# Kernel tuning notes

Measured on AMD Instinct MI355X. Metric: run time of the kernel, lower is better.

Reference implementation:

```python
import jax, jax.numpy as jnp
import numpy as np

VOCAB = 32000
DIM = 1024
DFF = 4096
NLLM = 3
B, S = 2, 2048
THRESH = 0.98
EPS = 1e-8


def setup_inputs() -> dict:
    key = jax.random.key(0)
    ks = jax.random.split(key, 5)
    x = jax.random.randint(ks[0], (B, S), 0, VOCAB)
    emb = 0.02 * jax.random.normal(ks[1], (VOCAB, DIM), jnp.float32)
    ln_g = jnp.ones((NLLM, DIM), jnp.float32)
    ln_b = jnp.zeros((NLLM, DIM), jnp.float32)
    W1 = 0.002 * jax.random.normal(ks[2], (NLLM, DIM, DFF), jnp.float32)
    b1 = jnp.zeros((NLLM, DFF), jnp.float32)
    W2 = 0.002 * jax.random.normal(ks[3], (NLLM, DFF, DIM), jnp.float32)
    b2 = jnp.zeros((NLLM, DIM), jnp.float32)
    W_out = (1.0 / np.sqrt(DIM)) * jax.random.normal(ks[4], (VOCAB, DIM), jnp.float32)
    return dict(x=x, emb=emb, ln_g=ln_g, ln_b=ln_b, W1=W1, b1=b1, W2=W2, b2=b2, W_out=W_out)


def _layernorm(h, g, b):
    m = jnp.mean(h, axis=-1, keepdims=True)
    v = jnp.var(h, axis=-1, keepdims=True)
    return (h - m) * jax.lax.rsqrt(v + 1e-5) * g + b


def reference(x, emb, ln_g, ln_b, W1, b1, W2, b2, W_out):
    # Cascaded early-exit ensemble. The torch code physically re-packs surviving
    # tokens; since each LLM block here is per-token (residual MLP), a masked
    # formulation computes identical per-token math and is jit-compatible.
    Bb, Ss = x.shape
    T = Bb * Ss
    h = emb[x.reshape(T)]                      # [T, D] token embeddings
    active = jnp.ones((T,), dtype=bool)
    final = jnp.zeros((T, VOCAB), dtype=h.dtype)
    for i in range(NLLM):                      # fixed, small number of LLMs
        hn = _layernorm(h, ln_g[i], ln_b[i])
        mlp = jax.nn.gelu(hn @ W1[i] + b1[i]) @ W2[i] + b2[i]
        h_out = h + mlp                        # [T, D]
        logits = h_out @ W_out.T               # [T, V] shared output head
        cos = jnp.sum(h * h_out, axis=-1) / (
            jnp.linalg.norm(h, axis=-1) * jnp.linalg.norm(h_out, axis=-1) + EPS)
        is_last = (i == NLLM - 1)
        should_exit = cos >= THRESH
        take = active if is_last else (active & should_exit)
        final = jnp.where(take[:, None], logits, final)   # scatter logits for exiting tokens
        active = active & (~take)
        h = jnp.where(active[:, None], h_out, h)          # continuing tokens carry h_out forward
    return final.reshape(Bb, Ss, VOCAB)
```

## Files before the change

kernel.cpp:

```cpp
#include <hip/hip_runtime.h>
#include <hip/hip_bf16.h>
#include <stdint.h>

constexpr int TK   = 4096;
constexpr int DIMC = 1024;
constexpr int DFFC = 4096;
constexpr int VOC  = 32000;
constexpr int NL   = 3;

typedef __attribute__((ext_vector_type(8))) short bf16x8;
typedef __attribute__((ext_vector_type(8))) _Float16 half8;
typedef __attribute__((ext_vector_type(4))) float f32x4;
using u16 = unsigned short;

__device__ __forceinline__ u16 f2bf(float f) {
  unsigned int u = __float_as_uint(f);
  u += 0x7FFF + ((u >> 16) & 1);
  return (u16)(u >> 16);
}

__device__ __forceinline__ void split16(float v, u16& hi, u16& lo) {
  _Float16 a = (_Float16)v;
  _Float16 b = (_Float16)(v - (float)a);
  hi = __builtin_bit_cast(u16, a);
  lo = __builtin_bit_cast(u16, b);
}

__device__ __forceinline__ float gelu_f(float x) {
  float x3 = x * x * x;
  return 0.5f * x * (1.0f + tanhf(0.7978845608028654f * (x + 0.044715f * x3)));
}

__device__ __forceinline__ void gll16(const void* g, void* l) {
  __builtin_amdgcn_global_load_lds(
      (const __attribute__((address_space(1))) unsigned int*)g,
      (__attribute__((address_space(3))) unsigned int*)l, 16, 0, 0);
}

__global__ __launch_bounds__(256) void k_init(const int* __restrict__ x,
    const float* __restrict__ emb, float* __restrict__ h,
    int* __restrict__ surv, int* __restrict__ cnts) {
  const int t = blockIdx.x, tid = threadIdx.x;
  if (t == 0 && tid < 16) cnts[tid] = (tid == 12) ? TK : 0;
  if (tid == 0) surv[t] = t;
  const int tok = x[t];
  ((float4*)(h + (size_t)t * DIMC))[tid] =
      ((const float4*)(emb + (size_t)tok * DIMC))[tid];
}

__global__ __launch_bounds__(256) void k_ln(const float* __restrict__ h,
    const int* __restrict__ surv, const int* __restrict__ pM,
    const float* __restrict__ g, const float* __restrict__ b,
    u16* __restrict__ hn1, u16* __restrict__ hn2) {
  const int bidx = blockIdx.x;
  if (bidx >= *pM) return;
  const int t = surv[bidx];
  const int tid = threadIdx.x;
  const int lane = tid & 63, wid = tid >> 6;
  __shared__ float sm[4];
  float4 v = ((const float4*)(h + (size_t)t * DIMC))[tid];
  float s = v.x + v.y + v.z + v.w;
#pragma unroll
  for (int o = 32; o; o >>= 1) s += __shfl_down(s, o);
  if (lane == 0) sm[wid] = s;
  __syncthreads();
  const float mean = (sm[0] + sm[1] + sm[2] + sm[3]) * (1.0f / DIMC);
  __syncthreads();
  float4 d;
  d.x = v.x - mean; d.y = v.y - mean; d.z = v.z - mean; d.w = v.w - mean;
  float q = d.x * d.x + d.y * d.y + d.z * d.z + d.w * d.w;
#pragma unroll
  for (int o = 32; o; o >>= 1) q += __shfl_down(q, o);
  if (lane == 0) sm[wid] = q;
  __syncthreads();
  const float var = (sm[0] + sm[1] + sm[2] + sm[3]) * (1.0f / DIMC);
  const float rstd = 1.0f / sqrtf(var + 1e-5f);
  float4 gg = ((const float4*)g)[tid];
  float4 bb = ((const float4*)b)[tid];
  float o4[4];
  o4[0] = (d.x * rstd * gg.x + bb.x) * 16.f;
  o4[1] = (d.y * rstd * gg.y + bb.y) * 16.f;
  o4[2] = (d.z * rstd * gg.z + bb.z) * 16.f;
  o4[3] = (d.w * rstd * gg.w + bb.w) * 16.f;
  ushort4 u1, u2;
  split16(o4[0], u1.x, u2.x); split16(o4[1], u1.y, u2.y);
  split16(o4[2], u1.z, u2.z); split16(o4[3], u1.w, u2.w);
  ((ushort4*)(hn1 + (size_t)bidx * DIMC))[tid] = u1;
  ((ushort4*)(hn2 + (size_t)bidx * DIMC))[tid] = u2;
}

__global__ __launch_bounds__(256) void k_splitw(const float* __restrict__ W,
    int K, int N, u16* __restrict__ O1, u16* __restrict__ O2) {
  __shared__ float t[32][33];
  const int bk = blockIdx.x * 32, bn = blockIdx.y * 32;
  const int lx = threadIdx.x & 31, ly = threadIdx.x >> 5;
#pragma unroll
  for (int i = 0; i < 32; i += 8)
    t[ly + i][lx] = W[(size_t)(bk + ly + i) * N + bn + lx];
  __syncthreads();
#pragma unroll
  for (int i = 0; i < 32; i += 8) {
    float v = t[lx][ly + i] * 256.f;
    u16 h1, h2; split16(v, h1, h2);
    const size_t o = (size_t)(bn + ly + i) * K + bk + lx;
    O1[o] = h1; O2[o] = h2;
  }
}

__global__ __launch_bounds__(256) void k_cvtb(const float* __restrict__ in,
    u16* __restrict__ o, int n4) {
  int i = blockIdx.x * blockDim.x + threadIdx.x;
  const int stride = gridDim.x * blockDim.x;
  for (; i < n4; i += stride) {
    float4 v = ((const float4*)in)[i];
    ushort4 u;
    u.x = f2bf(v.x); u.y = f2bf(v.y); u.z = f2bf(v.z); u.w = f2bf(v.w);
    ((ushort4*)o)[i] = u;
  }
}

template<int EPI, int LDK>
__global__ __launch_bounds__(256, 2) void k_mlp(
    const u16* __restrict__ wsb,
    int offA, int pstrA,
    int offB, int pstrB,
    const int* __restrict__ pM, int Kpart,
    const float* __restrict__ bias,
    u16* __restrict__ O1, u16* __restrict__ O2,
    float* __restrict__ PO, float osc)
{
  const int x = blockIdx.x & 7, g = blockIdx.x >> 3;
  const int rb = g & 31;
  int cb, z;
  if constexpr (EPI == 0) {
    cb = x * 4 + (g >> 5); z = 0;
  } else {
    const int cz = x * 2 + (g >> 5);
    cb = cz & 7; z = cz >> 3;
  }
  const int M = *pM;
  if (rb * 128 >= M) return;
  const int n0 = cb * 128;
  const int kz = z * Kpart;

  __shared__ u16 S[4 * 8192];
  const int tid = threadIdx.x, w = tid >> 6, l = tid & 63;
  const int lr16 = l & 15, hi = l >> 4;

  int offT;
  if (w == 0) offT = offA;
  else if (w == 1) offT = offA + pstrA;
  else if (w == 2) offT = offB;
  else offT = offB + pstrB;
  const int row0 = (w < 2) ? (rb * 128) : n0;
  const int gbase = offT + (row0 + lr16) * LDK + kz + hi * 8;

  const int wr = w >> 1, wc = w & 1;
  f32x4 acc[4][4];
#pragma unroll
  for (int mi = 0; mi < 4; ++mi)
#pragma unroll
    for (int ni = 0; ni < 4; ++ni) acc[mi][ni] = (f32x4){0.f, 0.f, 0.f, 0.f};

  const int NT = Kpart / 64;
  for (int kt = 0; kt < NT; ++kt) {
    __syncthreads();
#pragma unroll
    for (int s = 0; s < 16; ++s) {
      const int j = s >> 1, ks = s & 1;
      gll16(wsb + (size_t)(gbase + j * 16 * LDK + ks * 32 + kt * 64),
            (void*)&S[w * 8192 + (j * 2 + ks) * 512]);
    }
    __syncthreads();
#pragma unroll
    for (int ks = 0; ks < 2; ++ks) {
      half8 a1v[4], a2v[4], b1v[4], b2v[4];
#pragma unroll
      for (int mi = 0; mi < 4; ++mi) {
        const int sub = ((wr * 4 + mi) * 2 + ks) * 512 + l * 8;
        a1v[mi] = *(const half8*)&S[sub];
        a2v[mi] = *(const half8*)&S[8192 + sub];
      }
#pragma unroll
      for (int ni = 0; ni < 4; ++ni) {
        const int sub = ((wc * 4 + ni) * 2 + ks) * 512 + l * 8;
        b1v[ni] = *(const half8*)&S[16384 + sub];
        b2v[ni] = *(const half8*)&S[24576 + sub];
      }
      __builtin_amdgcn_s_setprio(1);
#pragma unroll
      for (int mi = 0; mi < 4; ++mi)
#pragma unroll
        for (int ni = 0; ni < 4; ++ni) {
          f32x4 c = acc[mi][ni];
          c = __builtin_amdgcn_mfma_f32_16x16x32_f16(a2v[mi], b1v[ni], c, 0, 0, 0);
          c = __builtin_amdgcn_mfma_f32_16x16x32_f16(a1v[mi], b2v[ni], c, 0, 0, 0);
          c = __builtin_amdgcn_mfma_f32_16x16x32_f16(a1v[mi], b1v[ni], c, 0, 0, 0);
          acc[mi][ni] = c;
        }
      __builtin_amdgcn_s_setprio(0);
    }
  }

#pragma unroll
  for (int mi = 0; mi < 4; ++mi)
#pragma unroll
    for (int ni = 0; ni < 4; ++ni) {
      const int n = n0 + wc * 64 + ni * 16 + lr16;
#pragma unroll
      for (int r = 0; r < 4; ++r) {
        const int m = rb * 128 + wr * 64 + mi * 16 + hi * 4 + r;
        float v = acc[mi][ni][r] * osc;
        if constexpr (EPI == 0) {
          v = gelu_f(v + bias[n]) * 64.f;
          u16 h1, h2; split16(v, h1, h2);
          O1[(size_t)m * DFFC + n] = h1;
          O2[(size_t)m * DFFC + n] = h2;
        } else {
          PO[(size_t)(z * TK + m) * DIMC + n] = v;
        }
      }
    }
}

__global__ __launch_bounds__(256) void k_decide(
    float* __restrict__ h, const float* __restrict__ p,
    const float* __restrict__ bias,
    const int* __restrict__ surv_in, int* __restrict__ surv_out,
    const int* __restrict__ pM, int* __restrict__ cnts,
    int* __restrict__ exit_idx, u16* __restrict__ hexit,
    int stage)
{
  const int bidx = blockIdx.x;
  if (bidx >= *pM) return;
  const int t = surv_in[bidx];
  const int tid = threadIdx.x;
  const int lane = tid & 63, wid = tid >> 6;
  __shared__ float sm[12];
  __shared__ int sif[2];
  float4 a  = ((const float4*)(h + (size_t)t * DIMC))[tid];
  float4 p0 = ((const float4*)(p + (size_t)bidx * DIMC))[tid];
  float4 p1 = ((const float4*)(p + (size_t)(TK + bidx) * DIMC))[tid];
  float4 bb = ((const float4*)bias)[tid];
  float4 o;
  o.x = a.x + p0.x + p1.x + bb.x;
  o.y = a.y + p0.y + p1.y + bb.y;
  o.z = a.z + p0.z + p1.z + bb.z;
  o.w = a.w + p0.w + p1.w + bb.w;
  float hh = a.x * a.x + a.y * a.y + a.z * a.z + a.w * a.w;
  float ho = a.x * o.x + a.y * o.y + a.z * o.z + a.w * o.w;
  float oo = o.x * o.x + o.y * o.y + o.z * o.z + o.w * o.w;
#pragma unroll
  for (int off = 32; off; off >>= 1) {
    hh += __shfl_down(hh, off);
    ho += __shfl_down(ho, off);
    oo += __shfl_down(oo, off);
  }
  if (lane == 0) { sm[wid] = hh; sm[4 + wid] = ho; sm[8 + wid] = oo; }
  __syncthreads();
  if (tid == 0) {
    int take;
    if (stage == NL - 1) take = 1;
    else {
      const float HH = sm[0] + sm[1] + sm[2] + sm[3];
      const float HO = sm[4] + sm[5] + sm[6] + sm[7];
      const float OO = sm[8] + sm[9] + sm[10] + sm[11];
      const float cosv = HO / (sqrtf(HH) * sqrtf(OO) + 1e-8f);
      take = (cosv >= 0.98f) ? 1 : 0;
    }
    int pos;
    if (take) {
      pos = atomicAdd(&cnts[stage], 1);
      exit_idx[pos] = t;
    } else {
      pos = atomicAdd(&cnts[4 + stage], 1);
      surv_out[pos] = t;
    }
    sif[0] = take; sif[1] = pos;
  }
  __syncthreads();
  if (sif[0]) {
    u16* dst = hexit + (size_t)sif[1] * DIMC;
    ushort4 u;
    u.x = f2bf(o.x); u.y = f2bf(o.y); u.z = f2bf(o.z); u.w = f2bf(o.w);
    ((ushort4*)dst)[tid] = u;
  } else {
    ((float4*)(h + (size_t)t * DIMC))[tid] = o;
  }
}

__global__ __launch_bounds__(512, 4) void k_logits(
    const u16* __restrict__ wsb, int offA, int offB,
    const int* __restrict__ pcnt,
    const int* __restrict__ exit_idx,
    float* __restrict__ out)
{
  const int x = blockIdx.x & 7, g = blockIdx.x >> 3;
  const int rb = g & 15;
  const int cb = x * 32 + (g >> 4);
  if (cb >= VOC / 128) return;
  const int cnt = *pcnt;
  if (rb * 256 >= cnt) return;
  const int n0 = cb * 128;

  __shared__ u16 S[2][12288];
  const int tid = threadIdx.x, w = tid >> 6, l = tid & 63;
  const int lr16 = l & 15, hi = l >> 4;

  int goff[3], loff[3];
#pragma unroll
  for (int q = 0; q < 3; ++q) {
    const int bi = w * 3 + q;
    if (bi < 16) {
      goff[q] = offA + (rb * 256 + bi * 16 + lr16) * DIMC + hi * 8;
      loff[q] = bi * 512;
    } else {
      const int j = bi - 16;
      goff[q] = offB + (n0 + j * 16 + lr16) * DIMC + hi * 8;
      loff[q] = 8192 + j * 512;
    }
  }

  const int wr = w >> 1, wc = w & 1;
  f32x4 acc[4][4];
#pragma unroll
  for (int mi = 0; mi < 4; ++mi)
#pragma unroll
    for (int ni = 0; ni < 4; ++ni) acc[mi][ni] = (f32x4){0.f, 0.f, 0.f, 0.f};

  auto STAGE = [&](int buf, int kt) {
#pragma unroll
    for (int q = 0; q < 3; ++q)
      gll16(wsb + (size_t)(goff[q] + kt * 32), (void*)&S[buf][loff[q]]);
  };

  STAGE(0, 0);
  STAGE(1, 1);
  const int NT = DIMC / 32;
  for (int kt = 0; kt < NT; ++kt) {
    const int cur = kt & 1;
    if (kt + 1 < NT) asm volatile("s_waitcnt vmcnt(3)" ::: "memory");
    else             asm volatile("s_waitcnt vmcnt(0)" ::: "memory");
    __builtin_amdgcn_s_barrier();
    bf16x8 aF[4], bF[4];
#pragma unroll
    for (int mi = 0; mi < 4; ++mi)
      aF[mi] = *(const bf16x8*)&S[cur][(wr * 4 + mi) * 512 + l * 8];
#pragma unroll
    for (int ni = 0; ni < 4; ++ni)
      bF[ni] = *(const bf16x8*)&S[cur][8192 + (wc * 4 + ni) * 512 + l * 8];
    __builtin_amdgcn_s_setprio(1);
#pragma unroll
    for (int mi = 0; mi < 4; ++mi)
#pragma unroll
      for (int ni = 0; ni < 4; ++ni)
        acc[mi][ni] = __builtin_amdgcn_mfma_f32_16x16x32_bf16(aF[mi], bF[ni], acc[mi][ni], 0, 0, 0);
    __builtin_amdgcn_s_setprio(0);
    asm volatile("s_waitcnt lgkmcnt(0)" ::: "memory");
    __builtin_amdgcn_s_barrier();
    if (kt + 2 < NT) STAGE(cur, kt + 2);
  }

  const int mvalid = cnt - rb * 256;
#pragma unroll
  for (int mi = 0; mi < 4; ++mi)
#pragma unroll
    for (int r = 0; r < 4; ++r) {
      const int mrow = wr * 64 + mi * 16 + hi * 4 + r;
      if (mrow < mvalid) {
        const int tok = exit_idx[rb * 256 + mrow];
        float* orow = out + (size_t)tok * VOC + n0 + wc * 64 + lr16;
#pragma unroll
        for (int ni = 0; ni < 4; ++ni)
          __builtin_nontemporal_store(acc[mi][ni][r], &orow[ni * 16]);
      }
    }
}

extern "C" void kernel_launch(void* const* d_in, const int* in_sizes, int n_in,
                              void* d_out, int out_size, void* d_ws, size_t ws_size,
                              hipStream_t stream)
{
  const int*   x    = (const int*)d_in[0];
  const float* emb  = (const float*)d_in[1];
  const float* ln_g = (const float*)d_in[2];
  const float* ln_b = (const float*)d_in[3];
  const float* W1   = (const float*)d_in[4];
  const float* b1   = (const float*)d_in[5];
  const float* W2   = (const float*)d_in[6];
  const float* b2   = (const float*)d_in[7];
  const float* Wout = (const float*)d_in[8];
  float* out = (float*)d_out;

  char* p = (char*)d_ws;
  size_t off = 0;
  auto alloc = [&](size_t bytes) -> void* {
    void* r = p + off;
    off += (bytes + 255) & ~(size_t)255;
    return r;
  };
  u16* wsb = (u16*)d_ws;
  float* h    = (float*)alloc((size_t)TK * DIMC * 4);
  float* pbuf = (float*)alloc((size_t)2 * TK * DIMC * 4);
  u16* hn1 = (u16*)pbuf;
  u16* hn2 = hn1 + (size_t)TK * DIMC;
  u16* act1 = (u16*)alloc((size_t)2 * TK * DFFC * 2);
  u16* act2 = act1 + (size_t)TK * DFFC;
  u16* Woutb = (u16*)alloc((size_t)VOC * DIMC * 2);
  u16* Wt = (u16*)alloc((size_t)2 * DFFC * DIMC * 2);
  u16* hexit = (u16*)alloc((size_t)TK * DIMC * 2);
  int* exit_idx = (int*)alloc((size_t)TK * 4);
  int* surv_a   = (int*)alloc((size_t)TK * 4);
  int* surv_b   = (int*)alloc((size_t)TK * 4);
  int* cnts     = (int*)alloc(64 * 4);

  const int offHn  = (int)(hn1  - wsb);
  const int offAct = (int)(act1 - wsb);
  const int offWob = (int)(Woutb- wsb);
  const int offWt  = (int)(Wt   - wsb);
  const int offHex = (int)(hexit- wsb);
  const int pstrHn  = TK * DIMC;
  const int pstrAct = TK * DFFC;
  const int pstrW   = DFFC * DIMC;

  k_init<<<TK, 256, 0, stream>>>(x, emb, h, surv_a, cnts);
  k_cvtb<<<2048, 256, 0, stream>>>(Wout, Woutb, VOC * DIMC / 4);
  int* surv_in  = surv_a;
  int* surv_out = surv_b;
  for (int i = 0; i < NL; ++i) {
    const int* pM = (i == 0) ? (cnts + 12) : (cnts + 4 + (i - 1));
    k_ln<<<TK, 256, 0, stream>>>(h, surv_in, pM, ln_g + i * DIMC, ln_b + i * DIMC, hn1, hn2);
    k_splitw<<<dim3(DIMC / 32, DFFC / 32), 256, 0, stream>>>(
        W1 + (size_t)i * DIMC * DFFC, DIMC, DFFC, Wt, Wt + (size_t)DFFC * DIMC);
    k_mlp<0, DIMC><<<1024, 256, 0, stream>>>(
        wsb, offHn, pstrHn, offWt, pstrW, pM, DIMC,
        b1 + (size_t)i * DFFC, act1, act2, nullptr, 1.f / 4096.f);
    k_splitw<<<dim3(DFFC / 32, DIMC / 32), 256, 0, stream>>>(
        W2 + (size_t)i * DFFC * DIMC, DFFC, DIMC, Wt, Wt + (size_t)DIMC * DFFC);
    k_mlp<1, DFFC><<<512, 256, 0, stream>>>(
        wsb, offAct, pstrAct, offWt, pstrW, pM, DFFC / 2,
        nullptr, nullptr, nullptr, pbuf, 1.f / 16384.f);
    k_decide<<<TK, 256, 0, stream>>>(h, pbuf, b2 + (size_t)i * DIMC,
        surv_in, surv_out, pM, cnts, exit_idx, hexit, i);
    k_logits<<<4096, 512, 0, stream>>>(wsb, offHex, offWob, cnts + i, exit_idx, out);
    int* tmp = surv_in; surv_in = surv_out; surv_out = tmp;
  }
}
```

Baseline: 1.461 ms.

## Double-buffer MLP GEMM shared-memory loads and vectorize weight split-transpose

The MLP GEMM kernel moves from a single 64-wide K stage with two full barriers to a double-buffered 32-wide K pipeline. The next tile's global-to-LDS loads are issued while MFMAs run on the current buffer, synchronised with explicit vmcnt/lgkmcnt waits and raw barriers. The weight split/transpose kernel now uses 64x64 tiles and writes ushort4 vectors instead of scalar u16 stores. This aims to hide load latency and cut store transactions, at the cost of more barriers per K step and delicate hand-written waitcnt ordering.

```diff
diff --git a/kernel.cpp b/kernel.cpp
--- a/kernel.cpp
+++ b/kernel.cpp
@@ -91,19 +91,28 @@
 
 __global__ __launch_bounds__(256) void k_splitw(const float* __restrict__ W,
     int K, int N, u16* __restrict__ O1, u16* __restrict__ O2) {
-  __shared__ float t[32][33];
-  const int bk = blockIdx.x * 32, bn = blockIdx.y * 32;
-  const int lx = threadIdx.x & 31, ly = threadIdx.x >> 5;
-#pragma unroll
-  for (int i = 0; i < 32; i += 8)
+  __shared__ float t[64][65];
+  const int bk = blockIdx.x * 64, bn = blockIdx.y * 64;
+  const int lx = threadIdx.x & 63, ly = threadIdx.x >> 6;
+#pragma unroll
+  for (int i = 0; i < 64; i += 4)
     t[ly + i][lx] = W[(size_t)(bk + ly + i) * N + bn + lx];
   __syncthreads();
-#pragma unroll
-  for (int i = 0; i < 32; i += 8) {
-    float v = t[lx][ly + i] * 256.f;
-    u16 h1, h2; split16(v, h1, h2);
-    const size_t o = (size_t)(bn + ly + i) * K + bk + lx;
-    O1[o] = h1; O2[o] = h2;
+  const int n4 = threadIdx.x >> 4;
+  const int kq = (threadIdx.x & 15) * 4;
+#pragma unroll
+  for (int j = 0; j < 4; ++j) {
+    const int n = j * 16 + n4;
+    ushort4 h1, h2;
+    {
+      float v0 = t[kq + 0][n] * 256.f, v1 = t[kq + 1][n] * 256.f;
+      float v2 = t[kq + 2][n] * 256.f, v3 = t[kq + 3][n] * 256.f;
+      split16(v0, h1.x, h2.x); split16(v1, h1.y, h2.y);
+      split16(v2, h1.z, h2.z); split16(v3, h1.w, h2.w);
+    }
+    const size_t o = (size_t)(bn + n) * K + bk + kq;
+    *(ushort4*)&O1[o] = h1;
+    *(ushort4*)&O2[o] = h2;
   }
 }
 
@@ -143,7 +152,7 @@
   const int n0 = cb * 128;
   const int kz = z * Kpart;
 
-  __shared__ u16 S[4 * 8192];
+  __shared__ u16 S[2][16384];
   const int tid = threadIdx.x, w = tid >> 6, l = tid & 63;
   const int lr16 = l & 15, hi = l >> 4;
 
@@ -153,7 +162,10 @@
   else if (w == 2) offT = offB;
   else offT = offB + pstrB;
   const int row0 = (w < 2) ? (rb * 128) : n0;
-  const int gbase = offT + (row0 + lr16) * LDK + kz + hi * 8;
+  int goff[8];
+#pragma unroll
+  for (int j = 0; j < 8; ++j)
+    goff[j] = offT + (row0 + j * 16 + lr16) * LDK + kz + hi * 8;
 
   const int wr = w >> 1, wc = w & 1;
   f32x4 acc[4][4];
@@ -162,44 +174,48 @@
 #pragma unroll
     for (int ni = 0; ni < 4; ++ni) acc[mi][ni] = (f32x4){0.f, 0.f, 0.f, 0.f};
 
-  const int NT = Kpart / 64;
+  auto STAGE = [&](int buf, int kt) {
+#pragma unroll
+    for (int j = 0; j < 8; ++j)
+      gll16(wsb + (size_t)(goff[j] + kt * 32), (void*)&S[buf][w * 4096 + j * 512]);
+  };
+
+  STAGE(0, 0);
+  STAGE(1, 1);
+  const int NT = Kpart / 32;
   for (int kt = 0; kt < NT; ++kt) {
-    __syncthreads();
-#pragma unroll
-    for (int s = 0; s < 16; ++s) {
-      const int j = s >> 1, ks = s & 1;
-      gll16(wsb + (size_t)(gbase + j * 16 * LDK + ks * 32 + kt * 64),
-            (void*)&S[w * 8192 + (j * 2 + ks) * 512]);
-    }
-    __syncthreads();
-#pragma unroll
-    for (int ks = 0; ks < 2; ++ks) {
-      half8 a1v[4], a2v[4], b1v[4], b2v[4];
-#pragma unroll
-      for (int mi = 0; mi < 4; ++mi) {
-        const int sub = ((wr * 4 + mi) * 2 + ks) * 512 + l * 8;
-        a1v[mi] = *(const half8*)&S[sub];
-        a2v[mi] = *(const half8*)&S[8192 + sub];
+    const int cur = kt & 1;
+    if (kt + 1 < NT) asm volatile("s_waitcnt vmcnt(8)" ::: "memory");
+    else             asm volatile("s_waitcnt vmcnt(0)" ::: "memory");
+    __builtin_amdgcn_s_barrier();
+    half8 a1v[4], a2v[4], b1v[4], b2v[4];
+#pragma unroll
+    for (int mi = 0; mi < 4; ++mi) {
+      const int sub = (wr * 4 + mi) * 512 + l * 8;
+      a1v[mi] = *(const half8*)&S[cur][sub];
+      a2v[mi] = *(const half8*)&S[cur][4096 + sub];
+    }
+#pragma unroll
+    for (int ni = 0; ni < 4; ++ni) {
+      const int sub = (wc * 4 + ni) * 512 + l * 8;
+      b1v[ni] = *(const half8*)&S[cur][8192 + sub];
+      b2v[ni] = *(const half8*)&S[cur][12288 + sub];
+    }
+    __builtin_amdgcn_s_setprio(1);
+#pragma unroll
+    for (int mi = 0; mi < 4; ++mi)
+#pragma unroll
+      for (int ni = 0; ni < 4; ++ni) {
+        f32x4 c = acc[mi][ni];
+        c = __builtin_amdgcn_mfma_f32_16x16x32_f16(a2v[mi], b1v[ni], c, 0, 0, 0);
+        c = __builtin_amdgcn_mfma_f32_16x16x32_f16(a1v[mi], b2v[ni], c, 0, 0, 0);
+        c = __builtin_amdgcn_mfma_f32_16x16x32_f16(a1v[mi], b1v[ni], c, 0, 0, 0);
+        acc[mi][ni] = c;
       }
-#pragma unroll
-      for (int ni = 0; ni < 4; ++ni) {
-        const int sub = ((wc * 4 + ni) * 2 + ks) * 512 + l * 8;
-        b1v[ni] = *(const half8*)&S[16384 + sub];
-        b2v[ni] = *(const half8*)&S[24576 + sub];
-      }
-      __builtin_amdgcn_s_setprio(1);
-#pragma unroll
-      for (int mi = 0; mi < 4; ++mi)
-#pragma unroll
-        for (int ni = 0; ni < 4; ++ni) {
-          f32x4 c = acc[mi][ni];
-          c = __builtin_amdgcn_mfma_f32_16x16x32_f16(a2v[mi], b1v[ni], c, 0, 0, 0);
-          c = __builtin_amdgcn_mfma_f32_16x16x32_f16(a1v[mi], b2v[ni], c, 0, 0, 0);
-          c = __builtin_amdgcn_mfma_f32_16x16x32_f16(a1v[mi], b1v[ni], c, 0, 0, 0);
-          acc[mi][ni] = c;
-        }
-      __builtin_amdgcn_s_setprio(0);
-    }
+    __builtin_amdgcn_s_setprio(0);
+    asm volatile("s_waitcnt lgkmcnt(0)" ::: "memory");
+    __builtin_amdgcn_s_barrier();
+    if (kt + 2 < NT) STAGE(cur, kt + 2);
   }
 
 #pragma unroll
@@ -430,12 +446,12 @@
   for (int i = 0; i < NL; ++i) {
     const int* pM = (i == 0) ? (cnts + 12) : (cnts + 4 + (i - 1));
     k_ln<<<TK, 256, 0, stream>>>(h, surv_in, pM, ln_g + i * DIMC, ln_b + i * DIMC, hn1, hn2);
-    k_splitw<<<dim3(DIMC / 32, DFFC / 32), 256, 0, stream>>>(
+    k_splitw<<<dim3(DIMC / 64, DFFC / 64), 256, 0, stream>>>(
         W1 + (size_t)i * DIMC * DFFC, DIMC, DFFC, Wt, Wt + (size_t)DFFC * DIMC);
     k_mlp<0, DIMC><<<1024, 256, 0, stream>>>(
         wsb, offHn, pstrHn, offWt, pstrW, pM, DIMC,
         b1 + (size_t)i * DFFC, act1, act2, nullptr, 1.f / 4096.f);
-    k_splitw<<<dim3(DFFC / 32, DIMC / 32), 256, 0, stream>>>(
+    k_splitw<<<dim3(DFFC / 64, DIMC / 64), 256, 0, stream>>>(
         W2 + (size_t)i * DFFC * DIMC, DFFC, DIMC, Wt, Wt + (size_t)DIMC * DFFC);
     k_mlp<1, DFFC><<<512, 256, 0, stream>>>(
         wsb, offAct, pstrAct, offWt, pstrW, pM, DFFC / 2,
```

After: 1.415 ms. 1.03x faster.
